# Performance work log

Hardware: AMD Instinct MI355X
Metric: run time of the kernel (lower is better)

The kernel has to match this reference:

```python
import jax, jax.numpy as jnp
import numpy as np
import math

D = 1024
B, S = 4, 4096


def setup_inputs() -> dict:
    key = jax.random.key(0)
    ks = jax.random.split(key, 8)
    x = jax.random.normal(ks[0], (B, S, D), dtype=jnp.float32)
    W_omega = jax.random.normal(ks[1], (D, D), dtype=jnp.float32) * (1.0 / math.sqrt(D))
    b_omega = jnp.zeros((D,), dtype=jnp.float32)
    log_scale = jnp.full((D,), math.log(0.1), dtype=jnp.float32)
    ln_gamma = jnp.ones((4 * D,), dtype=jnp.float32)
    ln_beta = jnp.zeros((4 * D,), dtype=jnp.float32)
    W1 = jax.random.normal(ks[2], (4 * D, 2 * D), dtype=jnp.float32) * (1.0 / math.sqrt(4 * D))
    b1 = jnp.zeros((2 * D,), dtype=jnp.float32)
    W2 = jax.random.normal(ks[3], (2 * D, D), dtype=jnp.float32) * (1.0 / math.sqrt(2 * D))
    b2 = jnp.zeros((D,), dtype=jnp.float32)
    return {"x": x, "W_omega": W_omega, "b_omega": b_omega, "log_scale": log_scale,
            "ln_gamma": ln_gamma, "ln_beta": ln_beta, "W1": W1, "b1": b1, "W2": W2, "b2": b2}


def _layernorm(x, gamma, beta, eps=1e-5):
    mu = jnp.mean(x, axis=-1, keepdims=True)
    var = jnp.var(x, axis=-1, keepdims=True)
    return (x - mu) * jax.lax.rsqrt(var + eps) * gamma + beta


def reference(x, W_omega, b_omega, log_scale, ln_gamma, ln_beta, W1, b1, W2, b2):
    # x: (B, S, D)
    seq_len = x.shape[1]
    omega = jnp.einsum('bsd,de->bse', x, W_omega) + b_omega
    position = jnp.arange(1, seq_len + 1, dtype=x.dtype)[None, :, None]  # (1,S,1)
    pos_scale = 1.0 / jnp.sqrt(position)
    scale = jnp.exp(log_scale)
    omega_scaled = omega * scale * pos_scale
    phi = jnp.cumsum(omega_scaled, axis=1)
    cos_phi = jnp.cos(phi)
    sin_phi = jnp.sin(phi)
    content_real = x * cos_phi
    content_imag = x * sin_phi
    mem_real = jnp.cumsum(content_real, axis=1) / position
    mem_imag = jnp.cumsum(content_imag, axis=1) / position
    retrieved_real = mem_real * cos_phi + mem_imag * sin_phi
    retrieved_imag = mem_imag * cos_phi - mem_real * sin_phi
    context = jnp.concatenate([content_real, content_imag, retrieved_real, retrieved_imag], axis=-1)
    h = _layernorm(context, ln_gamma, ln_beta)
    h = jnp.einsum('bsf,fg->bsg', h, W1) + b1
    h = jax.nn.gelu(h, approximate=False)  # torch GELU default is exact erf
    # dropout is identity in eval mode
    phase_contribution = jnp.einsum('bsg,gd->bsd', h, W2) + b2
    return x + phase_contribution
```

## Files before the change

### kernel.cpp

```cpp
#include <hip/hip_runtime.h>
#include <hip/hip_bf16.h>
#include <math.h>

typedef __hip_bfloat16 bf16;
typedef __attribute__((ext_vector_type(8))) short bf16x8;
typedef __attribute__((ext_vector_type(4))) float f32x4;

static constexpr int DD = 1024;
static constexpr int BB = 4;
static constexpr int SS = 4096;
static constexpr int FD = 4096;
static constexpr int GDIM = 2048;
static constexpr long SD = (long)SS * DD;
static constexpr long SD4 = 4 * SD;

__device__ __forceinline__ void gl2lds16(const bf16* g, bf16* l) {
    __builtin_amdgcn_global_load_lds(
        (const __attribute__((address_space(1))) void*)g,
        (__attribute__((address_space(3))) void*)l, 16, 0, 0);
}

__device__ __forceinline__ float gelu_exact(float v) {
    const float ax = fabsf(v) * 0.70710678118654752f;
    const float t = 1.0f / (1.0f + 0.3275911f * ax);
    const float poly = t * (0.254829592f + t * (-0.284496736f +
                       t * (1.421413741f + t * (-1.453152027f + t * 1.061405429f))));
    const float er = 1.0f - poly * __expf(-ax * ax);
    const float erfv = v < 0.f ? -er : er;
    return 0.5f * v * (1.0f + erfv);
}

__device__ __forceinline__ float bf2f(unsigned short us) {
    return __uint_as_float(((unsigned)us) << 16);
}

template <int EPI>
__global__ __launch_bounds__(512, 2) void gemm256(
    const bf16* __restrict__ A, const bf16* __restrict__ BT, void* __restrict__ Cp,
    const float* __restrict__ bias, const float* __restrict__ Xadd,
    const float2* __restrict__ is2, const float* __restrict__ uArr,
    const float* __restrict__ tArr,
    int M, int N, int K, long strA, long strBT, long strC)
{
    extern __shared__ bf16 lds[];
    const int tid = threadIdx.x;
    const int l = tid & 63, wv = tid >> 6;
    const int wr = wv >> 2, wc = wv & 3;

    int lin = blockIdx.y * gridDim.x + blockIdx.x;
    {
        const int nwg = gridDim.x * gridDim.y;
        const int qq = nwg >> 3, rr = nwg & 7;
        const int xcd = lin & 7, idx = lin >> 3;
        lin = (xcd < rr ? xcd * (qq + 1) : rr * (qq + 1) + (xcd - rr) * qq) + idx;
    }
    const long m0 = (long)(lin / gridDim.x) * 256;
    const long n0 = (long)(lin % gridDim.x) * 256;

    A += (long)blockIdx.z * strA;
    BT += (long)blockIdx.z * strBT;

    const int schunk = (tid & 3) ^ ((tid >> 3) & 3);
    const bf16* pa = A + (m0 + (tid >> 2)) * (long)K + schunk * 8;
    const bf16* pb = BT + (n0 + (tid >> 2)) * (long)K + schunk * 8;
    const long rowK = 128L * (long)K;
    const int stgOff = wv * 512;

    const int fm = l & 15, q = l >> 4;
    const int lof = fm * 32 + ((q ^ ((fm >> 1) & 3)) * 8);

    f32x4 acc[8][4];
#pragma unroll
    for (int i = 0; i < 8; ++i)
#pragma unroll
        for (int j = 0; j < 4; ++j) acc[i][j] = (f32x4){0.f, 0.f, 0.f, 0.f};

    const int NT = K >> 6;

    {
        bf16* dA0 = lds + stgOff;
        bf16* dA1 = lds + 8192 + stgOff;
        bf16* dB0 = lds + 32768 + stgOff;
        bf16* dB1 = lds + 40960 + stgOff;
        gl2lds16(pa, dA0);       gl2lds16(pa + rowK, dA0 + 4096);
        gl2lds16(pb, dB0);       gl2lds16(pb + rowK, dB0 + 4096);
        gl2lds16(pa + 32, dA1);  gl2lds16(pa + 32 + rowK, dA1 + 4096);
        gl2lds16(pb + 32, dB1);  gl2lds16(pb + 32 + rowK, dB1 + 4096);
        asm volatile("s_waitcnt vmcnt(4)" ::: "memory");
        __builtin_amdgcn_s_barrier();
    }

    for (int t = 0; t < NT; ++t) {
        const int buf = t & 1;
        const bool more = (t + 1) < NT;
        const long ko = (long)(t + 1) * 64;
        const bf16* As0 = lds + buf * 16384;
        const bf16* As1 = As0 + 8192;
        const bf16* Bs0 = lds + 32768 + buf * 16384;
        const bf16* Bs1 = Bs0 + 8192;
        bf16* nA0 = lds + (buf ^ 1) * 16384 + stgOff;
        bf16* nA1 = nA0 + 8192;
        bf16* nB0 = lds + 32768 + (buf ^ 1) * 16384 + stgOff;
        bf16* nB1 = nB0 + 8192;

        {
            const bf16* bb = Bs0 + (wc * 64) * 32 + lof;
            const bf16* ab = As0 + (wr * 128) * 32 + lof;
            bf16x8 bq[4], a0[4], a1[4];
#pragma unroll
            for (int j = 0; j < 4; ++j) bq[j] = *(const bf16x8*)(bb + j * 512);
#pragma unroll
            for (int i = 0; i < 4; ++i) a0[i] = *(const bf16x8*)(ab + i * 512);
#pragma unroll
            for (int i = 0; i < 4; ++i) a1[i] = *(const bf16x8*)(ab + 64 * 32 + i * 512);
            if (more) {
                gl2lds16(pa + ko, nA0); gl2lds16(pa + ko + rowK, nA0 + 4096);
                gl2lds16(pb + ko, nB0); gl2lds16(pb + ko + rowK, nB0 + 4096);
            }
            __builtin_amdgcn_s_setprio(1);
#pragma unroll
            for (int i = 0; i < 4; ++i)
#pragma unroll
                for (int j = 0; j < 4; ++j)
                    acc[i][j] = __builtin_amdgcn_mfma_f32_16x16x32_bf16(a0[i], bq[j], acc[i][j], 0, 0, 0);
            __builtin_amdgcn_s_setprio(0);
            if (more) { gl2lds16(pa + ko + 32, nA1); gl2lds16(pa + ko + 32 + rowK, nA1 + 4096); }
            __builtin_amdgcn_s_setprio(1);
#pragma unroll
            for (int i = 0; i < 4; ++i)
#pragma unroll
                for (int j = 0; j < 4; ++j)
                    acc[4 + i][j] = __builtin_amdgcn_mfma_f32_16x16x32_bf16(a1[i], bq[j], acc[4 + i][j], 0, 0, 0);
            __builtin_amdgcn_s_setprio(0);
        }
        if (more) asm volatile("s_waitcnt vmcnt(6)" ::: "memory");
        else      asm volatile("s_waitcnt vmcnt(0)" ::: "memory");
        __builtin_amdgcn_s_barrier();

        {
            const bf16* bb = Bs1 + (wc * 64) * 32 + lof;
            const bf16* ab = As1 + (wr * 128) * 32 + lof;
            bf16x8 bq[4], a0[4], a1[4];
#pragma unroll
            for (int j = 0; j < 4; ++j) bq[j] = *(const bf16x8*)(bb + j * 512);
#pragma unroll
            for (int i = 0; i < 4; ++i) a0[i] = *(const bf16x8*)(ab + i * 512);
#pragma unroll
            for (int i = 0; i < 4; ++i) a1[i] = *(const bf16x8*)(ab + 64 * 32 + i * 512);
            if (more) { gl2lds16(pb + ko + 32, nB1); gl2lds16(pb + ko + 32 + rowK, nB1 + 4096); }
            __builtin_amdgcn_s_setprio(1);
#pragma unroll
            for (int i = 0; i < 4; ++i)
#pragma unroll
                for (int j = 0; j < 4; ++j)
                    acc[i][j] = __builtin_amdgcn_mfma_f32_16x16x32_bf16(a0[i], bq[j], acc[i][j], 0, 0, 0);
            __builtin_amdgcn_s_setprio(0);
            __builtin_amdgcn_s_setprio(1);
#pragma unroll
            for (int i = 0; i < 4; ++i)
#pragma unroll
                for (int j = 0; j < 4; ++j)
                    acc[4 + i][j] = __builtin_amdgcn_mfma_f32_16x16x32_bf16(a1[i], bq[j], acc[4 + i][j], 0, 0, 0);
            __builtin_amdgcn_s_setprio(0);
        }
        if (more) {
            asm volatile("s_waitcnt vmcnt(4)" ::: "memory");
            __builtin_amdgcn_s_barrier();
        }
    }

    const long cb = (long)blockIdx.z * strC;
    float uu[4], tb[4];
    if (EPI == 1) {
#pragma unroll
        for (int j = 0; j < 4; ++j) {
            const long col = n0 + wc * 64 + j * 16 + fm;
            uu[j] = uArr[col];
            tb[j] = tArr[col] + bias[col];
        }
    }
#pragma unroll
    for (int i = 0; i < 8; ++i) {
        const long rB = m0 + wr * 128 + i * 16 + q * 4;
#pragma unroll
        for (int r2 = 0; r2 < 4; ++r2) {
            const long row = rB + r2;
            float2 st;
            if (EPI == 1) st = is2[row];
#pragma unroll
            for (int j = 0; j < 4; ++j) {
                const long col = n0 + wc * 64 + j * 16 + fm;
                float v = acc[i][j][r2];
                if (EPI == 0) {
                    v += bias[row];
                    ((bf16*)Cp)[cb + row * (long)N + col] = __float2bfloat16(v);
                } else if (EPI == 1) {
                    v = st.x * v - st.y * uu[j] + tb[j];
                    v = gelu_exact(v);
                    ((bf16*)Cp)[cb + row * (long)N + col] = __float2bfloat16(v);
                } else {
                    v += bias[col] + Xadd[row * (long)N + col];
                    ((float*)Cp)[cb + row * (long)N + col] = v;
                }
            }
        }
    }
}

__global__ void conv_bf16(const float* __restrict__ in, bf16* __restrict__ out, long n) {
    long i = ((long)blockIdx.x * 256 + threadIdx.x) * 4;
    if (i >= n) return;
    const float4 v = *(const float4*)(in + i);
    bf16 o[4] = {__float2bfloat16(v.x), __float2bfloat16(v.y),
                 __float2bfloat16(v.z), __float2bfloat16(v.w)};
    *(uint2*)(out + i) = *(uint2*)o;
}

__global__ void transpose_f32_bf16(const float* __restrict__ in, bf16* __restrict__ out,
                                   int R, int C, long inStr, long outStr,
                                   const float* __restrict__ rscale) {
    __shared__ float tl[64][65];
    const float* ip = in + (long)blockIdx.z * inStr;
    bf16* op = out + (long)blockIdx.z * outStr;
    const int r0 = blockIdx.y * 64, c0 = blockIdx.x * 64;
    const int tr = threadIdx.x >> 6, tc = threadIdx.x & 63;
#pragma unroll
    for (int k = 0; k < 16; k++) {
        int r = k * 4 + tr;
        float v = ip[(long)(r0 + r) * C + c0 + tc];
        if (rscale) v *= rscale[r0 + r];
        tl[r][tc] = v;
    }
    __syncthreads();
#pragma unroll
    for (int k = 0; k < 16; k++) {
        int r = k * 4 + tr;
        op[(long)(c0 + r) * R + r0 + tc] = __float2bfloat16(tl[tc][r]);
    }
}

__global__ void zero_f32(float* p, int n) {
    int i = blockIdx.x * 256 + threadIdx.x;
    if (i < n) p[i] = 0.f;
}

__global__ void ut_kernel(const float* __restrict__ W1, const float* __restrict__ gamma,
                          const float* __restrict__ beta, float* __restrict__ uArr,
                          float* __restrict__ tArr) {
    const int g = blockIdx.x * 256 + threadIdx.x;
    const int f0 = blockIdx.y * 512;
    float su = 0.f, st = 0.f;
    for (int f = 0; f < 512; ++f) {
        const float w = W1[(long)(f0 + f) * GDIM + g];
        su += gamma[f0 + f] * w;
        st += beta[f0 + f] * w;
    }
    atomicAdd(&uArr[g], su);
    atomicAdd(&tArr[g], st);
}

__global__ __launch_bounds__(1024) void scan16(
    const bf16* __restrict__ omegaT, const bf16* __restrict__ xT,
    const float* __restrict__ log_scale, bf16* __restrict__ ctx,
    long strIn, long strCtx)
{
    __shared__ bf16 stg[64 * 70];
    const int tid = threadIdx.x;
    const int wv = tid >> 6, lane = tid & 63;
    const int d0 = blockIdx.x * 16;
    const int d = d0 + wv;
    const int z = blockIdx.z;
    const float sc = expf(log_scale[d]);
    const bf16* po = omegaT + (long)z * strIn + (long)d * SS;
    const bf16* px = xT + (long)z * strIn + (long)d * SS;
    bf16* pc = ctx + (long)z * strCtx;
    const int so_i = tid >> 4;
    const int so_d = tid & 15;

    float phi_c = 0.f, mr_c = 0.f, mi_c = 0.f;
    for (int tchunk = 0; tchunk < SS / 64; tchunk++) {
        const int s = tchunk * 64 + lane;
        const float pos = (float)(s + 1);
        float w = __bfloat162float(po[s]) * sc * rsqrtf(pos);
#pragma unroll
        for (int dlt = 1; dlt < 64; dlt <<= 1) {
            float v = __shfl_up(w, dlt, 64);
            if (lane >= dlt) w += v;
        }
        const float phi = phi_c + w;
        float sph, cph;
        sincosf(phi, &sph, &cph);
        const float xv = __bfloat162float(px[s]);
        const float cr = xv * cph, ci = xv * sph;
        float crs = cr, cis = ci;
#pragma unroll
        for (int dlt = 1; dlt < 64; dlt <<= 1) {
            float v1 = __shfl_up(crs, dlt, 64);
            float v2 = __shfl_up(cis, dlt, 64);
            if (lane >= dlt) { crs += v1; cis += v2; }
        }
        const float invp = 1.0f / pos;
        const float mr = (mr_c + crs) * invp;
        const float mi = (mi_c + cis) * invp;
        const float rr = mr * cph + mi * sph;
        const float ri = mi * cph - mr * sph;
        stg[lane * 70 +      wv] = __float2bfloat16(cr);
        stg[lane * 70 + 17 + wv] = __float2bfloat16(ci);
        stg[lane * 70 + 34 + wv] = __float2bfloat16(rr);
        stg[lane * 70 + 51 + wv] = __float2bfloat16(ri);
        phi_c += __shfl(w, 63, 64);
        mr_c += __shfl(crs, 63, 64);
        mi_c += __shfl(cis, 63, 64);
        __syncthreads();
        bf16* row = pc + (long)(tchunk * 64 + so_i) * FD + d0 + so_d;
        row[0]          = stg[so_i * 70 +      so_d];
        row[DD]         = stg[so_i * 70 + 17 + so_d];
        row[2 * DD]     = stg[so_i * 70 + 34 + so_d];
        row[3 * DD]     = stg[so_i * 70 + 51 + so_d];
        __syncthreads();
    }
}

__global__ __launch_bounds__(256) void stats2(
    const bf16* __restrict__ ctx, float2* __restrict__ is2, long strCtx)
{
    const int s = blockIdx.x * 4 + (threadIdx.x >> 6);
    const int lane = threadIdx.x & 63;
    const int z = blockIdx.z;
    const bf16* p = ctx + (long)z * strCtx + (long)s * FD;
    float sm = 0.f, sq = 0.f;
#pragma unroll
    for (int i = 0; i < 8; ++i) {
        bf16x8 v8 = *(const bf16x8*)(p + lane * 8 + i * 512);
#pragma unroll
        for (int j = 0; j < 8; ++j) {
            const float v = bf2f((unsigned short)v8[j]);
            sm += v;
            sq += v * v;
        }
    }
#pragma unroll
    for (int o = 1; o < 64; o <<= 1) {
        sm += __shfl_xor(sm, o, 64);
        sq += __shfl_xor(sq, o, 64);
    }
    if (lane == 0) {
        const float mu = sm * (1.0f / FD);
        const float var = sq * (1.0f / FD) - mu * mu;
        const float is = rsqrtf(var + 1e-5f);
        is2[z * SS + s] = make_float2(is, is * mu);
    }
}

extern "C" void kernel_launch(void* const* d_in, const int* in_sizes, int n_in,
                              void* d_out, int out_size, void* d_ws, size_t ws_size,
                              hipStream_t stream)
{
    const float* x = (const float*)d_in[0];
    const float* Wo = (const float*)d_in[1];
    const float* bo = (const float*)d_in[2];
    const float* lsc = (const float*)d_in[3];
    const float* gam = (const float*)d_in[4];
    const float* bet = (const float*)d_in[5];
    const float* W1 = (const float*)d_in[6];
    const float* b1 = (const float*)d_in[7];
    const float* W2 = (const float*)d_in[8];
    const float* b2 = (const float*)d_in[9];

    static bool attr_done = false;
    if (!attr_done) {
        hipFuncSetAttribute(reinterpret_cast<const void*>(gemm256<0>),
                            hipFuncAttributeMaxDynamicSharedMemorySize, 131072);
        hipFuncSetAttribute(reinterpret_cast<const void*>(gemm256<1>),
                            hipFuncAttributeMaxDynamicSharedMemorySize, 131072);
        hipFuncSetAttribute(reinterpret_cast<const void*>(gemm256<2>),
                            hipFuncAttributeMaxDynamicSharedMemorySize, 131072);
        attr_done = true;
    }

    char* ws = (char*)d_ws;
    const size_t MB = 1024 * 1024;

    bf16* W1gT = (bf16*)(ws + 0);
    bf16* W2T = (bf16*)(ws + 16 * MB);
    bf16* WoT = (bf16*)(ws + 20 * MB);
    float2* is2 = (float2*)(ws + 22 * MB);
    float* uArr = (float*)(ws + 22 * MB + 128 * 1024);
    float* tArr = (float*)(ws + 22 * MB + 136 * 1024);

    transpose_f32_bf16<<<dim3(DD / 64, DD / 64, 1), 256, 0, stream>>>(Wo, WoT, DD, DD, 0, 0, nullptr);
    transpose_f32_bf16<<<dim3(GDIM / 64, FD / 64, 1), 256, 0, stream>>>(W1, W1gT, FD, GDIM, 0, 0, gam);
    transpose_f32_bf16<<<dim3(DD / 64, GDIM / 64, 1), 256, 0, stream>>>(W2, W2T, GDIM, DD, 0, 0, nullptr);
    zero_f32<<<(2 * GDIM + 255) / 256, 256, 0, stream>>>(uArr, 2 * GDIM);
    ut_kernel<<<dim3(GDIM / 256, FD / 512, 1), 256, 0, stream>>>(W1, gam, bet, uArr, tArr);

    if (ws_size >= 220 * MB) {
        bf16* xT  = (bf16*)(ws + 23 * MB);
        bf16* omT = (bf16*)(ws + 55 * MB);
        bf16* ctx = (bf16*)(ws + 87 * MB);
        bf16* xb  = (bf16*)(ws + 87 * MB);
        bf16* h1  = (bf16*)(ws + 23 * MB);

        conv_bf16<<<(int)(BB * SD / 1024), 256, 0, stream>>>(x, xb, BB * SD);
        transpose_f32_bf16<<<dim3(DD / 64, SS / 64, BB), 256, 0, stream>>>(x, xT, SS, DD, SD, SD, nullptr);

        gemm256<0><<<dim3(SS / 256, DD / 256, BB), 512, 131072, stream>>>(
            WoT, xb, omT, bo, nullptr, nullptr, nullptr, nullptr, DD, SS, DD, 0L, SD, SD);

        scan16<<<dim3(DD / 16, 1, BB), 1024, 0, stream>>>(omT, xT, lsc, ctx, SD, SD4);

        stats2<<<dim3(SS / 4, 1, BB), 256, 0, stream>>>(ctx, is2, SD4);

        gemm256<1><<<dim3(GDIM / 256, BB * SS / 256, 1), 512, 131072, stream>>>(
            ctx, W1gT, h1, b1, nullptr, is2, uArr, tArr, BB * SS, GDIM, FD, 0L, 0L, 0L);

        gemm256<2><<<dim3(DD / 256, BB * SS / 256, 1), 512, 131072, stream>>>(
            h1, W2T, d_out, b2, x, nullptr, nullptr, nullptr, BB * SS, DD, GDIM, 0L, 0L, 0L);
    } else {
        bf16* xb  = (bf16*)(ws + 23 * MB);
        bf16* ctx = (bf16*)(ws + 23 * MB);
        bf16* omT = (bf16*)(ws + 55 * MB);
        bf16* xT  = (bf16*)(ws + 63 * MB);
        bf16* h1  = (bf16*)(ws + 55 * MB);

        for (int b = 0; b < BB; b++) {
            const float* xbf = x + (long)b * SD;
            conv_bf16<<<(int)(SD / 1024), 256, 0, stream>>>(xbf, xb, SD);
            transpose_f32_bf16<<<dim3(DD / 64, SS / 64, 1), 256, 0, stream>>>(xbf, xT, SS, DD, 0, 0, nullptr);
            gemm256<0><<<dim3(SS / 256, DD / 256, 1), 512, 131072, stream>>>(
                WoT, xb, omT, bo, nullptr, nullptr, nullptr, nullptr, DD, SS, DD, 0L, 0L, 0L);
            scan16<<<dim3(DD / 16, 1, 1), 1024, 0, stream>>>(omT, xT, lsc, ctx, 0L, 0L);
            stats2<<<dim3(SS / 4, 1, 1), 256, 0, stream>>>(ctx, is2, 0L);
            gemm256<1><<<dim3(GDIM / 256, SS / 256, 1), 512, 131072, stream>>>(
                ctx, W1gT, h1, b1, nullptr, is2, uArr, tArr, SS, GDIM, FD, 0L, 0L, 0L);
            gemm256<2><<<dim3(DD / 256, SS / 256, 1), 512, 131072, stream>>>(
                h1, W2T, (float*)d_out + (long)b * SD, b2, xbf, nullptr, nullptr, nullptr,
                SS, DD, GDIM, 0L, 0L, 0L);
        }
    }
}
```

Measured before the change: 764.2 us.

## Parallelize sequence scan across waves per channel and transpose context in place

Replaces the per-16-channel serial chunked scan with a kernel that gives each channel its own 512-thread block, splitting the sequence into 8 wave segments with a two-level scan (intra-wave shuffles plus cross-wave offsets via shared memory). Context is written channel-major with contiguous stores, then a new in-place pairwise 64x64 tile transpose kernel converts it back to the sequence-major layout the later kernels expect. This removes the long serial dependency over 64 chunks and the per-chunk barriers, at the cost of an extra full read and write of the context buffer.

```diff
diff --git a/kernel.cpp b/kernel.cpp
--- a/kernel.cpp
+++ b/kernel.cpp
@@ -259,65 +259,126 @@
     atomicAdd(&tArr[g], st);
 }
 
-__global__ __launch_bounds__(1024) void scan16(
+__global__ __launch_bounds__(512) void scan8(
     const bf16* __restrict__ omegaT, const bf16* __restrict__ xT,
     const float* __restrict__ log_scale, bf16* __restrict__ ctx,
     long strIn, long strCtx)
 {
-    __shared__ bf16 stg[64 * 70];
-    const int tid = threadIdx.x;
-    const int wv = tid >> 6, lane = tid & 63;
-    const int d0 = blockIdx.x * 16;
-    const int d = d0 + wv;
+    __shared__ float stA[8], stB[8], stC[8];
+    const int d = blockIdx.x;
     const int z = blockIdx.z;
+    const int wv = threadIdx.x >> 6, lane = threadIdx.x & 63;
     const float sc = expf(log_scale[d]);
     const bf16* po = omegaT + (long)z * strIn + (long)d * SS;
     const bf16* px = xT + (long)z * strIn + (long)d * SS;
-    bf16* pc = ctx + (long)z * strCtx;
-    const int so_i = tid >> 4;
-    const int so_d = tid & 15;
-
-    float phi_c = 0.f, mr_c = 0.f, mi_c = 0.f;
-    for (int tchunk = 0; tchunk < SS / 64; tchunk++) {
-        const int s = tchunk * 64 + lane;
+    bf16* pc = ctx + (long)z * strCtx + (long)d * SS;
+
+    const int s0 = wv * 512;
+    float phi_loc[8], xv[8], cph[8], sph[8], crs[8], cis[8];
+
+    float lphi = 0.f;
+#pragma unroll
+    for (int c = 0; c < 8; ++c) {
+        const int s = s0 + c * 64 + lane;
         const float pos = (float)(s + 1);
         float w = __bfloat162float(po[s]) * sc * rsqrtf(pos);
+        xv[c] = __bfloat162float(px[s]);
 #pragma unroll
         for (int dlt = 1; dlt < 64; dlt <<= 1) {
             float v = __shfl_up(w, dlt, 64);
             if (lane >= dlt) w += v;
         }
-        const float phi = phi_c + w;
-        float sph, cph;
-        sincosf(phi, &sph, &cph);
-        const float xv = __bfloat162float(px[s]);
-        const float cr = xv * cph, ci = xv * sph;
-        float crs = cr, cis = ci;
+        phi_loc[c] = lphi + w;
+        lphi += __shfl(w, 63, 64);
+    }
+    if (lane == 0) stA[wv] = lphi;
+    __syncthreads();
+    float phi_off = 0.f;
+#pragma unroll
+    for (int u = 0; u < 8; ++u) phi_off += (u < wv) ? stA[u] : 0.f;
+
+    float lcr = 0.f, lci = 0.f;
+#pragma unroll
+    for (int c = 0; c < 8; ++c) {
+        const float phi = phi_loc[c] + phi_off;
+        float sp, cp;
+        sincosf(phi, &sp, &cp);
+        cph[c] = cp; sph[c] = sp;
+        float a = xv[c] * cp, b = xv[c] * sp;
 #pragma unroll
         for (int dlt = 1; dlt < 64; dlt <<= 1) {
-            float v1 = __shfl_up(crs, dlt, 64);
-            float v2 = __shfl_up(cis, dlt, 64);
-            if (lane >= dlt) { crs += v1; cis += v2; }
-        }
-        const float invp = 1.0f / pos;
-        const float mr = (mr_c + crs) * invp;
-        const float mi = (mi_c + cis) * invp;
-        const float rr = mr * cph + mi * sph;
-        const float ri = mi * cph - mr * sph;
-        stg[lane * 70 +      wv] = __float2bfloat16(cr);
-        stg[lane * 70 + 17 + wv] = __float2bfloat16(ci);
-        stg[lane * 70 + 34 + wv] = __float2bfloat16(rr);
-        stg[lane * 70 + 51 + wv] = __float2bfloat16(ri);
-        phi_c += __shfl(w, 63, 64);
-        mr_c += __shfl(crs, 63, 64);
-        mi_c += __shfl(cis, 63, 64);
-        __syncthreads();
-        bf16* row = pc + (long)(tchunk * 64 + so_i) * FD + d0 + so_d;
-        row[0]          = stg[so_i * 70 +      so_d];
-        row[DD]         = stg[so_i * 70 + 17 + so_d];
-        row[2 * DD]     = stg[so_i * 70 + 34 + so_d];
-        row[3 * DD]     = stg[so_i * 70 + 51 + so_d];
-        __syncthreads();
+            float v1 = __shfl_up(a, dlt, 64);
+            float v2 = __shfl_up(b, dlt, 64);
+            if (lane >= dlt) { a += v1; b += v2; }
+        }
+        crs[c] = lcr + a;
+        cis[c] = lci + b;
+        lcr += __shfl(a, 63, 64);
+        lci += __shfl(b, 63, 64);
+    }
+    if (lane == 0) { stB[wv] = lcr; stC[wv] = lci; }
+    __syncthreads();
+    float roff = 0.f, ioff = 0.f;
+#pragma unroll
+    for (int u = 0; u < 8; ++u) {
+        roff += (u < wv) ? stB[u] : 0.f;
+        ioff += (u < wv) ? stC[u] : 0.f;
+    }
+
+#pragma unroll
+    for (int c = 0; c < 8; ++c) {
+        const int s = s0 + c * 64 + lane;
+        const float invp = 1.0f / (float)(s + 1);
+        const float mr = (crs[c] + roff) * invp;
+        const float mi = (cis[c] + ioff) * invp;
+        const float cp = cph[c], sp = sph[c];
+        const float cr = xv[c] * cp, ci = xv[c] * sp;
+        const float rr = mr * cp + mi * sp;
+        const float ri = mi * cp - mr * sp;
+        pc[s] = __float2bfloat16(cr);
+        pc[(long)DD * SS + s] = __float2bfloat16(ci);
+        pc[2L * DD * SS + s] = __float2bfloat16(rr);
+        pc[3L * DD * SS + s] = __float2bfloat16(ri);
+    }
+}
+
+__global__ __launch_bounds__(256) void tpair(bf16* __restrict__ ctx, long strCtx) {
+    __shared__ float tA[64][65];
+    __shared__ float tB[64][65];
+    const int z = blockIdx.z;
+    int rem = blockIdx.x, a = 0;
+    for (int i = 0; i < 64; i++) {
+        int cnt = 64 - i;
+        if (rem < cnt) { a = i; break; }
+        rem -= cnt;
+    }
+    const int b = a + rem;
+    bf16* base = ctx + (long)z * strCtx;
+    const int tr = threadIdx.x >> 6, tc = threadIdx.x & 63;
+#pragma unroll
+    for (int k = 0; k < 16; k++) {
+        int i = k * 4 + tr;
+        tA[i][tc] = __bfloat162float(base[(long)(a * 64 + i) * 4096 + b * 64 + tc]);
+    }
+    if (a != b) {
+#pragma unroll
+        for (int k = 0; k < 16; k++) {
+            int i = k * 4 + tr;
+            tB[i][tc] = __bfloat162float(base[(long)(b * 64 + i) * 4096 + a * 64 + tc]);
+        }
+    }
+    __syncthreads();
+#pragma unroll
+    for (int k = 0; k < 16; k++) {
+        int i = k * 4 + tr;
+        base[(long)(b * 64 + i) * 4096 + a * 64 + tc] = __float2bfloat16(tA[tc][i]);
+    }
+    if (a != b) {
+#pragma unroll
+        for (int k = 0; k < 16; k++) {
+            int i = k * 4 + tr;
+            base[(long)(a * 64 + i) * 4096 + b * 64 + tc] = __float2bfloat16(tB[tc][i]);
+        }
     }
 }
 
@@ -394,6 +455,8 @@
     zero_f32<<<(2 * GDIM + 255) / 256, 256, 0, stream>>>(uArr, 2 * GDIM);
     ut_kernel<<<dim3(GDIM / 256, FD / 512, 1), 256, 0, stream>>>(W1, gam, bet, uArr, tArr);
 
+    const int NPAIR = 64 * 65 / 2;
+
     if (ws_size >= 220 * MB) {
         bf16* xT  = (bf16*)(ws + 23 * MB);
         bf16* omT = (bf16*)(ws + 55 * MB);
@@ -407,7 +470,9 @@
         gemm256<0><<<dim3(SS / 256, DD / 256, BB), 512, 131072, stream>>>(
             WoT, xb, omT, bo, nullptr, nullptr, nullptr, nullptr, DD, SS, DD, 0L, SD, SD);
 
-        scan16<<<dim3(DD / 16, 1, BB), 1024, 0, stream>>>(omT, xT, lsc, ctx, SD, SD4);
+        scan8<<<dim3(DD, 1, BB), 512, 0, stream>>>(omT, xT, lsc, ctx, SD, SD4);
+
+        tpair<<<dim3(NPAIR, 1, BB), 256, 0, stream>>>(ctx, SD4);
 
         stats2<<<dim3(SS / 4, 1, BB), 256, 0, stream>>>(ctx, is2, SD4);
 
@@ -429,7 +494,8 @@
             transpose_f32_bf16<<<dim3(DD / 64, SS / 64, 1), 256, 0, stream>>>(xbf, xT, SS, DD, 0, 0, nullptr);
             gemm256<0><<<dim3(SS / 256, DD / 256, 1), 512, 131072, stream>>>(
                 WoT, xb, omT, bo, nullptr, nullptr, nullptr, nullptr, DD, SS, DD, 0L, 0L, 0L);
-            scan16<<<dim3(DD / 16, 1, 1), 1024, 0, stream>>>(omT, xT, lsc, ctx, 0L, 0L);
+            scan8<<<dim3(DD, 1, 1), 512, 0, stream>>>(omT, xT, lsc, ctx, 0L, 0L);
+            tpair<<<dim3(NPAIR, 1, 1), 256, 0, stream>>>(ctx, 0L);
             stats2<<<dim3(SS / 4, 1, 1), 256, 0, stream>>>(ctx, is2, 0L);
             gemm256<1><<<dim3(GDIM / 256, SS / 256, 1), 512, 131072, stream>>>(
                 ctx, W1gT, h1, b1, nullptr, is2, uArr, tArr, SS, GDIM, FD, 0L, 0L, 0L);
```

Measured after the change: 709.6 us. -7.1%, faster.
